# Performance work log

Measured on AMD Instinct MI355X. Metric: run time of the kernel, lower is better.

## Reference

```python
import jax, jax.numpy as jnp
import numpy as np

IMAGE_W = 1024
IMAGE_H = 1024
STRIDES = (8, 16, 32, 64, 128)
TOP_N = 1000
MIN_SCORE = 0.05
NMS_THR = 0.6
MAX_DET = 100
NEG = -1e9  # sentinel for suppressed scores


def _positions(stride):
    # Faithful to repo: shifts_x indexed by feature_h, shifts_y by feature_w,
    # grid built [hf, wf, 2] = [shift_x_i, shift_y_j], then permute(1,0,2).
    hf, wf = IMAGE_H // stride, IMAGE_W // stride
    sx = (jnp.arange(hf, dtype=jnp.float32) + 0.5) * stride
    sy = (jnp.arange(wf, dtype=jnp.float32) + 0.5) * stride
    pos = jnp.stack(jnp.meshgrid(sx, sy, indexing='ij'), axis=-1)  # [hf, wf, 2]
    return jnp.transpose(pos, (1, 0, 2)).reshape(-1, 2)  # [hf*wf, 2]


def _filter_level(cls_h, reg_h, ctr_h, pos):
    B, C = cls_h.shape[0], cls_h.shape[-1]
    cls_h = jax.nn.sigmoid(cls_h).reshape(B, -1, C)
    reg_h = jnp.exp(reg_h).reshape(B, -1, 4)
    ctr_h = jax.nn.sigmoid(ctr_h).reshape(B, -1)
    scores = jnp.max(cls_h, axis=-1)
    classes = jnp.argmax(cls_h, axis=-1).astype(jnp.int32)
    scores = jnp.sqrt(scores * ctr_h)
    N = scores.shape[1]
    if N >= TOP_N:
        scores, idx = jax.lax.top_k(scores, TOP_N)  # sorted descending, like torch.topk
        classes = jnp.take_along_axis(classes, idx, axis=1)
        reg_h = jnp.take_along_axis(reg_h, idx[..., None], axis=1)
        posb = pos[idx]  # [B, TOP_N, 2]
    else:
        posb = jnp.broadcast_to(pos[None], (B, N, 2))
    return scores, classes, reg_h, posb


def _snap(reg, pos):
    # reg: [B, N, 4] (l,t,r,b), pos: [B, N, 2]
    b = jnp.concatenate([pos - reg[:, :, 0:2], pos + reg[:, :, 2:4]], axis=-1)
    b = b.astype(jnp.int32)  # torch .int() truncation
    b = jnp.stack([
        jnp.maximum(b[..., 0], 0),
        jnp.maximum(b[..., 1], 0),
        jnp.minimum(b[..., 2], IMAGE_W - 1),
        jnp.minimum(b[..., 3], IMAGE_H - 1),
    ], axis=-1)
    return b.astype(jnp.float32)


def _nms_image(scores, classes, boxes):
    # scores [N], classes [N] int32, boxes [N,4] float (already snapped to int grid)
    s = jnp.where(scores > MIN_SCORE, scores, NEG)
    x1, y1, x2, y2 = boxes[:, 0], boxes[:, 1], boxes[:, 2], boxes[:, 3]
    areas = (x2 - x1) * (y2 - y1)
    out_s = -jnp.ones((MAX_DET,), jnp.float32)
    out_c = -jnp.ones((MAX_DET,), jnp.float32)
    out_b = -jnp.ones((MAX_DET, 4), jnp.float32)

    def body(i, st):
        s, os_, oc, ob = st
        idx = jnp.argmax(s)            # highest remaining score -> sorted keep order
        ok = s[idx] > MIN_SCORE        # any un-suppressed valid candidate left?
        bb = boxes[idx]
        iw = jnp.clip(jnp.minimum(x2, bb[2]) - jnp.maximum(x1, bb[0]), 0.0)
        ih = jnp.clip(jnp.minimum(y2, bb[3]) - jnp.maximum(y1, bb[1]), 0.0)
        inter = iw * ih
        iou = inter / (areas + areas[idx] - inter + 1e-12)
        s = jnp.where((iou > NMS_THR) & ok, NEG, s)
        s = s.at[idx].set(NEG)
        os_ = os_.at[i].set(jnp.where(ok, scores[idx], -1.0))
        oc = oc.at[i].set(jnp.where(ok, classes[idx].astype(jnp.float32), -1.0))
        ob = ob.at[i].set(jnp.where(ok, bb, -jnp.ones((4,), jnp.float32)))
        return (s, os_, oc, ob)

    _, os_, oc, ob = jax.lax.fori_loop(0, MAX_DET, body, (s, out_s, out_c, out_b))
    return os_, oc, ob


def _decode(cls_heads, reg_heads, ctr_heads):
    sc_l, cl_l, rg_l, ps_l = [], [], [], []
    for c, r, t, st in zip(cls_heads, reg_heads, ctr_heads, STRIDES):
        sc, cl, rg, ps = _filter_level(c, r, t, _positions(st))
        sc_l.append(sc); cl_l.append(cl); rg_l.append(rg); ps_l.append(ps)
    scores = jnp.concatenate(sc_l, axis=1)
    classes = jnp.concatenate(cl_l, axis=1)
    regs = jnp.concatenate(rg_l, axis=1)
    poss = jnp.concatenate(ps_l, axis=1)
    boxes = _snap(regs, poss)
    return jax.vmap(_nms_image)(scores, classes, boxes)


def setup_inputs() -> dict:
    key = jax.random.key(0)
    ks = jax.random.split(key, 15)
    B, C = 8, 80
    sizes = [IMAGE_H // s for s in STRIDES]
    inp = {}
    for i, hw in enumerate(sizes):
        inp[f'cls{i}'] = jax.random.normal(ks[i], (B, hw, hw, C), dtype=jnp.float32)
        # +3 so exp(reg) gives realistic ~20px extents
        inp[f'reg{i}'] = jax.random.normal(ks[5 + i], (B, hw, hw, 4), dtype=jnp.float32) + 3.0
        inp[f'ctr{i}'] = jax.random.normal(ks[10 + i], (B, hw, hw, 1), dtype=jnp.float32)
    return inp


def reference(cls0, cls1, cls2, cls3, cls4,
              reg0, reg1, reg2, reg3, reg4,
              ctr0, ctr1, ctr2, ctr3, ctr4):
    cls_heads = [cls0, cls1, cls2, cls3, cls4]
    reg_heads = [reg0, reg1, reg2, reg3, reg4]
    ctr_heads = [ctr0, ctr1, ctr2, ctr3, ctr4]
    batch_scores, batch_classes, batch_boxes = _decode(cls_heads, reg_heads, ctr_heads)
    return batch_scores, batch_classes, batch_boxes
```

## Files before the change

kernel.cpp:

```cpp
#include <hip/hip_runtime.h>

#define NPOS 21824
#define MINS 0.05f
#define BT2  256
#define NW2  4
#define TFAST 0.85f
#define CAP  16384
#define CNTSTRIDE 32

struct Ptrs { const float* cls[5]; const float* reg[5]; const float* ctr[5]; };

__device__ __forceinline__ float sigf(float x){ return 1.0f/(1.0f+expf(-x)); }

__device__ __forceinline__ void cstore_u32(unsigned* p, unsigned v){
    __hip_atomic_store(p, v, __ATOMIC_RELAXED, __HIP_MEMORY_SCOPE_AGENT);
}
__device__ __forceinline__ void cstore_i32(int* p, int v){
    __hip_atomic_store(p, v, __ATOMIC_RELAXED, __HIP_MEMORY_SCOPE_AGENT);
}
__device__ __forceinline__ void cstore_u64(unsigned long long* p, unsigned long long v){
    __hip_atomic_store(p, v, __ATOMIC_RELAXED, __HIP_MEMORY_SCOPE_AGENT);
}
__device__ __forceinline__ unsigned cload_u32(const unsigned* p){
    return __hip_atomic_load(p, __ATOMIC_RELAXED, __HIP_MEMORY_SCOPE_AGENT);
}
__device__ __forceinline__ int cload_i32(const int* p){
    return __hip_atomic_load(p, __ATOMIC_RELAXED, __HIP_MEMORY_SCOPE_AGENT);
}
__device__ __forceinline__ unsigned long long cload_u64(const unsigned long long* p){
    return __hip_atomic_load(p, __ATOMIC_RELAXED, __HIP_MEMORY_SCOPE_AGENT);
}

__device__ __forceinline__ unsigned long long mkkey(unsigned int b, int p){
    return ((unsigned long long)b << 16) | (unsigned)(65535 - p);
}

__device__ __forceinline__ float4 computeBox(const Ptrs& P, int img, int p){
    int base, lw, stride, lvl;
    if (p < 16384)      { lvl=0; base=0;     lw=7; stride=8;   }
    else if (p < 20480) { lvl=1; base=16384; lw=6; stride=16;  }
    else if (p < 21504) { lvl=2; base=20480; lw=5; stride=32;  }
    else if (p < 21760) { lvl=3; base=21504; lw=4; stride=64;  }
    else                { lvl=4; base=21760; lw=3; stride=128; }
    int pl = p - base;
    int h = pl >> lw, w = pl & ((1<<lw)-1);
    long long lidx = (long long)img*(1<<(2*lw)) + pl;
    float4 rg = ((const float4*)P.reg[lvl])[lidx];
    float x = (w + 0.5f)*(float)stride;
    float y = (h + 0.5f)*(float)stride;
    int ix1 = (int)(x - expf(rg.x));
    int iy1 = (int)(y - expf(rg.y));
    int ix2 = (int)(x + expf(rg.z));
    int iy2 = (int)(y + expf(rg.w));
    ix1 = max(ix1,0); iy1 = max(iy1,0);
    ix2 = min(ix2,1023); iy2 = min(iy2,1023);
    return make_float4((float)ix1,(float)iy1,(float)ix2,(float)iy2);
}

__device__ void suffix_pick(const int* hist, int* wsum, int K,
                            unsigned int prefBase, int shift,
                            unsigned int* shPref, int* shK, int tid)
{
    const int g = 2048 / BT2;
    int lo = tid*g, ls = 0;
#pragma unroll
    for (int q = 0; q < g; ++q) ls += hist[lo + q];
    int lane = tid & 63, wv = tid >> 6;
    int v = ls;
#pragma unroll
    for (int off = 1; off < 64; off <<= 1) {
        int o = __shfl_down(v, off);
        if (lane + off < 64) v += o;
    }
    if (lane == 0) wsum[wv] = v;
    __syncthreads();
    int add = 0;
    for (int q = wv + 1; q < NW2; ++q) add += wsum[q];
    int mine = v + add;
    int above = mine - ls;
    if (above < K && mine >= K) {
        int cum = above;
        for (int b = lo + g - 1; b >= lo; --b) {
            cum += hist[b];
            if (cum >= K) {
                *shPref = prefBase | ((unsigned)b << shift);
                *shK = K - (cum - hist[b]);
                break;
            }
        }
    }
    __syncthreads();
}

__global__ __launch_bounds__(BT2) void k_all(Ptrs P, float* scoreAll, int* clsAll,
                                             unsigned long long* list, int* listCnt,
                                             int* done, float* out)
{
    __shared__ __align__(16) unsigned long long sRow[256][4];
    __shared__ int wsum[NW2];
    __shared__ unsigned int shPref;
    __shared__ int shK, tick, eqn;
    __shared__ unsigned long long eqKey[256];
    __shared__ unsigned long long sel[256];
    __shared__ unsigned long long sorted[256];
    __shared__ float4 sBox[256];
    __shared__ float  sCls[256];
    __shared__ int accIdx[100];
    __shared__ float4 accBox[100];
    __shared__ int shNaM, shNa;
    __shared__ unsigned long long shLast;
    __shared__ int lcnt, lbase, myOrder;

    int* hist = (int*)&sRow[0][0];

    int tid = threadIdx.x;
    int img = blockIdx.y;
    int blk = blockIdx.x;

    {
        int posb = tid >> 2;
        int l    = tid & 3;
        int p    = blk*64 + posb;
        int lvl, base, lw;
        if (blk < 256)      { lvl=0; base=0;     lw=7; }
        else if (blk < 320) { lvl=1; base=16384; lw=6; }
        else if (blk < 336) { lvl=2; base=20480; lw=5; }
        else if (blk < 340) { lvl=3; base=21504; lw=4; }
        else                { lvl=4; base=21760; lw=3; }
        int pl = p - base;
        long long lidx = (long long)img*(1<<(2*lw)) + pl;

        if (tid == 0) lcnt = 0;
        __syncthreads();

        const float4* c4 = (const float4*)(P.cls[lvl] + lidx*80);
        float mx = -3.4e38f; int mi = 0;
#pragma unroll
        for (int j = 0; j < 5; ++j) {
            int k = j*4 + l;
            float4 v = c4[k];
            int cb = k*4;
            if (v.x > mx){mx=v.x; mi=cb;}
            if (v.y > mx){mx=v.y; mi=cb+1;}
            if (v.z > mx){mx=v.z; mi=cb+2;}
            if (v.w > mx){mx=v.w; mi=cb+3;}
        }
#pragma unroll
        for (int d = 1; d < 4; d <<= 1) {
            float omx = __shfl_xor(mx, d);
            int   omi = __shfl_xor(mi, d);
            if (omx > mx || (omx == mx && omi < mi)) { mx = omx; mi = omi; }
        }
        int myTicket = -1;
        unsigned long long myKey = 0;
        if (l == 0) {
            float ct = P.ctr[lvl][lidx];
            float sc = sqrtf(sigf(mx)*sigf(ct));
            int o = img*NPOS + p;
            cstore_u32((unsigned*)scoreAll + o, __float_as_uint(sc));
            cstore_i32(clsAll + o, mi);
            if (sc > TFAST) {
                myTicket = atomicAdd(&lcnt, 1);
                myKey = mkkey(__float_as_uint(sc), p);
            }
        }
        __syncthreads();
        if (tid == 0) lbase = lcnt ? atomicAdd(&listCnt[img*CNTSTRIDE], lcnt) : 0;
        __syncthreads();
        if (myTicket >= 0) {
            int t = lbase + myTicket;
            if (t < CAP) cstore_u64(list + (long long)img*CAP + t, myKey);
        }
    }

    __syncthreads();
    if (tid == 0)
        myOrder = __hip_atomic_fetch_add(&done[img*CNTSTRIDE], 1,
                                         __ATOMIC_RELAXED, __HIP_MEMORY_SCOPE_AGENT);
    __syncthreads();
    if (myOrder != 340) return;

    const unsigned int* gs = (const unsigned int*)scoreAll + (long long)img*NPOS;
    const int* gCls = clsAll + (long long)img*NPOS;
    const unsigned long long* gl = list + (long long)img*CAP;

    float* outS = out + img*100;
    float* outC = out + 800 + img*100;
    float* outB = out + 1600 + img*400;

    int cnt = cload_i32(&listCnt[img*CNTSTRIDE]);
    bool fastPath = (cnt >= 256 && cnt <= CAP);

    for (int i = tid; i < 2048; i += BT2) hist[i] = 0;
    if (tid == 0) { tick = 0; eqn = 0; }
    __syncthreads();

    unsigned int kth; int need;
    if (fastPath) {
        for (int i = tid; i < cnt; i += BT2)
            atomicAdd(&hist[(unsigned)(cload_u64(gl + i) >> 35)], 1);
        __syncthreads();
        suffix_pick(hist, wsum, 256, 0u, 19, &shPref, &shK, tid);
        unsigned int pref = shPref; int K2 = shK;
        for (int i = tid; i < 2048; i += BT2) hist[i] = 0;
        __syncthreads();
        for (int i = tid; i < cnt; i += BT2) {
            unsigned long long k = cload_u64(gl + i);
            if ((unsigned)(k >> 35) == (pref >> 19))
                atomicAdd(&hist[(unsigned)(k >> 24) & 2047], 1);
        }
        __syncthreads();
        suffix_pick(hist, wsum, K2, pref, 8, &shPref, &shK, tid);
        kth = shPref >> 8; need = shK;
        for (int i = tid; i < cnt; i += BT2) {
            unsigned long long k = cload_u64(gl + i);
            unsigned int hb = (unsigned)(k >> 24);
            if (hb > kth)       { int t = atomicAdd(&tick, 1); sel[t] = k; }
            else if (hb == kth) { int t = atomicAdd(&eqn, 1); if (t < 256) eqKey[t] = k; }
        }
    } else {
        for (int i = tid; i < NPOS; i += BT2)
            atomicAdd(&hist[cload_u32(gs + i) >> 19], 1);
        __syncthreads();
        suffix_pick(hist, wsum, 256, 0u, 19, &shPref, &shK, tid);
        unsigned int pref = shPref; int K2 = shK;
        for (int i = tid; i < 2048; i += BT2) hist[i] = 0;
        __syncthreads();
        for (int i = tid; i < NPOS; i += BT2) {
            unsigned int b = cload_u32(gs + i);
            if ((b >> 19) == (pref >> 19)) atomicAdd(&hist[(b >> 8) & 2047], 1);
        }
        __syncthreads();
        suffix_pick(hist, wsum, K2, pref, 8, &shPref, &shK, tid);
        kth = shPref >> 8; need = shK;
        for (int i = tid; i < NPOS; i += BT2) {
            unsigned int b = cload_u32(gs + i), hb = b >> 8;
            if (hb > kth)       { int t = atomicAdd(&tick, 1); sel[t] = mkkey(b, i); }
            else if (hb == kth) { int t = atomicAdd(&eqn, 1); if (t < 256) eqKey[t] = mkkey(b, i); }
        }
    }
    __syncthreads();
    int m = eqn, nG = tick;
    if (m <= 256) {
        for (int q = tid; q < m; q += BT2) {
            unsigned long long kq = eqKey[q];
            int r = 0;
            for (int j = 0; j < m; ++j) r += (eqKey[j] > kq);
            if (r < need) sel[nG + r] = kq;
        }
    } else if (tid == 0) {
        unsigned long long last = ~0ULL;
        for (int c = 0; c < need; ++c) {
            unsigned long long best = 0;
            if (fastPath) {
                for (int i = 0; i < cnt; ++i) {
                    unsigned long long k2 = cload_u64(gl + i);
                    if ((unsigned)(k2 >> 24) == kth && k2 < last && k2 > best) best = k2;
                }
            } else {
                for (int i = 0; i < NPOS; ++i) {
                    unsigned int b = cload_u32(gs + i);
                    if ((b >> 8) == kth) {
                        unsigned long long k2 = mkkey(b, i);
                        if (k2 < last && k2 > best) best = k2;
                    }
                }
            }
            sel[nG + c] = best; last = best;
        }
    }
    __syncthreads();

    {
        unsigned long long k = sel[tid];
        int r = 0;
        for (int j = 0; j < 256; ++j) r += (sel[j] > k);
        sorted[r] = k;
    }
    __syncthreads();
    {
        int p = 65535 - (int)(sorted[tid] & 0xFFFF);
        sBox[tid] = computeBox(P, img, p);
        sCls[tid] = (float)cload_i32(gCls + p);
    }

    float myScore = __uint_as_float((unsigned int)(sorted[tid] >> 16));
    int nValid = __syncthreads_count(myScore > MINS ? 1 : 0);

    {
        float4 bi = sBox[tid];
        float  ai = (bi.z-bi.x)*(bi.w-bi.y);
#pragma unroll
        for (int qq = 0; qq < 4; ++qq) {
            unsigned long long mv = 0;
#pragma unroll 8
            for (int jj = 0; jj < 64; ++jj) {
                int j = qq*64 + jj;
                float4 bj = sBox[j];
                float aj = (bj.z-bj.x)*(bj.w-bj.y);
                float iw = fmaxf(fminf(bj.z,bi.z)-fmaxf(bj.x,bi.x),0.f);
                float ih = fmaxf(fminf(bj.w,bi.w)-fmaxf(bj.y,bi.y),0.f);
                float in_ = iw*ih;
                bool s = (j > tid) && (in_/(aj+ai-in_+1e-12f) > 0.6f);
                mv |= ((unsigned long long)s) << jj;
            }
            sRow[tid][qq] = mv;
        }
    }
    __syncthreads();

    if (tid == 0) {
        int na = 0;
        unsigned long long r0=0, r1=0, r2=0, r3=0;
#define FCOS_WBLK(RW, IB)                                                  \
        {                                                                  \
            int hi = nValid < ((IB)+1)*64 ? nValid : ((IB)+1)*64;          \
            for (int i = (IB)*64; i < hi && na < 100; ++i) {               \
                if ((RW >> (i - (IB)*64)) & 1ull) continue;                \
                accIdx[na++] = i;                                          \
                const ulonglong2* rp = (const ulonglong2*)sRow[i];         \
                ulonglong2 ra = rp[0], rb = rp[1];                         \
                r0 |= ra.x; r1 |= ra.y; r2 |= rb.x; r3 |= rb.y;            \
            }                                                              \
        }
        FCOS_WBLK(r0,0) FCOS_WBLK(r1,1) FCOS_WBLK(r2,2) FCOS_WBLK(r3,3)
#undef FCOS_WBLK
        shNaM = na; shNa = na;
    }
    __syncthreads();

    int naM = shNaM;
    if (naM < 100 && nValid == 256) {
        if (tid < naM) accBox[tid] = sBox[accIdx[tid]];
        if (tid == 0) shLast = sorted[255];
        __syncthreads();
        while (true) {
            if (shNa >= 100) break;
            unsigned long long last = shLast;
            unsigned long long bk = 0;
            for (int i = tid; i < NPOS; i += BT2) {
                unsigned long long k2 = mkkey(cload_u32(gs + i), i);
                if (k2 < last && k2 > bk) bk = k2;
            }
#pragma unroll
            for (int off = 32; off > 0; off >>= 1) {
                unsigned long long o = __shfl_down(bk, off);
                if (o > bk) bk = o;
            }
            int lane = tid & 63, wv = tid >> 6;
            if (lane == 0) eqKey[wv] = bk;
            __syncthreads();
            if (tid == 0) {
                unsigned long long best = 0;
                for (int q = 0; q < NW2; ++q) if (eqKey[q] > best) best = eqKey[q];
                shLast = best;
            }
            __syncthreads();
            unsigned long long ck = shLast;
            if (ck == 0ULL) break;
            float sc = __uint_as_float((unsigned int)(ck >> 16));
            if (!(sc > MINS)) break;
            int p = 65535 - (int)(ck & 0xFFFF);
            float4 bb = computeBox(P, img, p);
            float ba = (bb.z-bb.x)*(bb.w-bb.y);
            int na = shNa;
            bool mySup = false;
            if (tid < na) {
                float4 ab = accBox[tid];
                float aa = (ab.z-ab.x)*(ab.w-ab.y);
                float iw = fmaxf(fminf(bb.z,ab.z)-fmaxf(bb.x,ab.x),0.f);
                float ih = fmaxf(fminf(bb.w,ab.w)-fmaxf(bb.y,ab.y),0.f);
                float in_ = iw*ih;
                mySup = in_/(ba+aa-in_+1e-12f) > 0.6f;
            }
            int supCnt = __syncthreads_count(mySup);
            if (supCnt == 0) {
                if (tid == 0) {
                    int na2 = shNa;
                    outS[na2] = sc;
                    outC[na2] = (float)cload_i32(gCls + p);
                    outB[4*na2+0]=bb.x; outB[4*na2+1]=bb.y;
                    outB[4*na2+2]=bb.z; outB[4*na2+3]=bb.w;
                    accBox[na2] = bb;
                    shNa = na2 + 1;
                }
            }
            __syncthreads();
        }
    }
    __syncthreads();

    {
        int naM2 = shNaM, naT = shNa;
        if (tid < 100) {
            if (tid < naM2) {
                int r = accIdx[tid];
                unsigned long long k = sorted[r];
                float4 b = sBox[r];
                outS[tid] = __uint_as_float((unsigned int)(k >> 16));
                outC[tid] = sCls[r];
                outB[4*tid+0]=b.x; outB[4*tid+1]=b.y;
                outB[4*tid+2]=b.z; outB[4*tid+3]=b.w;
            } else if (tid >= naT) {
                outS[tid] = -1.f; outC[tid] = -1.f;
                outB[4*tid+0]=-1.f; outB[4*tid+1]=-1.f;
                outB[4*tid+2]=-1.f; outB[4*tid+3]=-1.f;
            }
        }
    }
}

extern "C" void kernel_launch(void* const* d_in, const int* in_sizes, int n_in,
                              void* d_out, int out_size, void* d_ws, size_t ws_size,
                              hipStream_t stream) {
    Ptrs P;
    bool interleaved = (in_sizes[1] == 8 * 128 * 128 * 4);
    for (int i = 0; i < 5; ++i) {
        if (interleaved) {
            P.cls[i] = (const float*)d_in[3*i];
            P.reg[i] = (const float*)d_in[3*i + 1];
            P.ctr[i] = (const float*)d_in[3*i + 2];
        } else {
            P.cls[i] = (const float*)d_in[i];
            P.reg[i] = (const float*)d_in[5 + i];
            P.ctr[i] = (const float*)d_in[10 + i];
        }
    }

    char* wbase = (char*)d_ws;
    size_t off = 0;
    auto alloc = [&](size_t bytes) -> void* {
        void* r = wbase + off;
        off += (bytes + 255) & ~(size_t)255;
        return r;
    };
    float*              scoreAll = (float*)alloc((size_t)8 * NPOS * 4);
    int*                clsAll   = (int*)alloc((size_t)8 * NPOS * 4);
    unsigned long long* list     = (unsigned long long*)alloc((size_t)8 * CAP * 8);
    int*                listCnt  = (int*)alloc((size_t)8 * CNTSTRIDE * 4);
    int*                done     = (int*)alloc((size_t)8 * CNTSTRIDE * 4);

    hipMemsetAsync(listCnt, 0, 2 * 8 * CNTSTRIDE * sizeof(int), stream);

    dim3 gA(341, 8);
    k_all<<<gA, BT2, 0, stream>>>(P, scoreAll, clsAll, list, listCnt, done,
                                  (float*)d_out);
}
```

Before: 178.4 us.

## Shard per-image candidate counters and completion tickets into 8 sectors

Splits the single per-image candidate-list counter and done-counter into 8 sector counters (blocks assigned by blk&7), with a two-level completion ticket that picks the last block per image. This is meant to reduce contention on global atomics across the 341 blocks per image. The final block then compacts the sector lists into a shared-memory buffer so the radix-select passes read LDS instead of repeated global atomic loads. Shared-memory buffers are aliased to fit, and the fast path now requires at most 3072 total candidates and 2048 per sector.

```diff
diff --git a/kernel.cpp b/kernel.cpp
--- a/kernel.cpp
+++ b/kernel.cpp
@@ -5,8 +5,11 @@
 #define BT2  256
 #define NW2  4
 #define TFAST 0.85f
-#define CAP  16384
-#define CNTSTRIDE 32
+#define SEC  8
+#define SCAP 2048
+#define CAP  (SEC*SCAP)
+#define SLCAP 3072
+#define CSTRIDE 32
 
 struct Ptrs { const float* cls[5]; const float* reg[5]; const float* ctr[5]; };
 
@@ -93,29 +96,34 @@
 }
 
 __global__ __launch_bounds__(BT2) void k_all(Ptrs P, float* scoreAll, int* clsAll,
-                                             unsigned long long* list, int* listCnt,
-                                             int* done, float* out)
+                                             unsigned long long* list, int* secCnt,
+                                             int* dSec, int* dImg, float* out)
 {
-    __shared__ __align__(16) unsigned long long sRow[256][4];
+    __shared__ __align__(16) unsigned long long slist[SLCAP];
+    __shared__ int hist[2048];
+    __shared__ unsigned long long sel[256];
+    __shared__ unsigned long long eqKey[256];
     __shared__ int wsum[NW2];
+    __shared__ int cntS[SEC], offS[SEC+1];
     __shared__ unsigned int shPref;
     __shared__ int shK, tick, eqn;
-    __shared__ unsigned long long eqKey[256];
-    __shared__ unsigned long long sel[256];
-    __shared__ unsigned long long sorted[256];
-    __shared__ float4 sBox[256];
-    __shared__ float  sCls[256];
-    __shared__ int accIdx[100];
-    __shared__ float4 accBox[100];
-    __shared__ int shNaM, shNa;
+    __shared__ int shNaM, shNa, shTotal, shMaxS;
     __shared__ unsigned long long shLast;
-    __shared__ int lcnt, lbase, myOrder;
-
-    int* hist = (int*)&sRow[0][0];
+    __shared__ int lcnt, lbase, lastFlag;
+
+    unsigned long long* sorted = (unsigned long long*)((char*)slist + 0);
+    float4* sBox  = (float4*)((char*)slist + 2048);
+    float*  sCls  = (float*)((char*)slist + 6144);
+    int*    accIdx= (int*)((char*)slist + 7168);
+    float4* accBox= (float4*)((char*)slist + 7680);
+    unsigned long long (*sRow)[4] =
+        (unsigned long long (*)[4])((char*)slist + 9472);
 
     int tid = threadIdx.x;
     int img = blockIdx.y;
     int blk = blockIdx.x;
+    int s   = blk & 7;
+    int ssz = (s < 5) ? 43 : 42;
 
     {
         int posb = tid >> 2;
@@ -165,20 +173,29 @@
             }
         }
         __syncthreads();
-        if (tid == 0) lbase = lcnt ? atomicAdd(&listCnt[img*CNTSTRIDE], lcnt) : 0;
+        if (tid == 0)
+            lbase = lcnt ? __hip_atomic_fetch_add(&secCnt[(img*SEC+s)*CSTRIDE], lcnt,
+                                __ATOMIC_RELAXED, __HIP_MEMORY_SCOPE_AGENT) : 0;
         __syncthreads();
         if (myTicket >= 0) {
             int t = lbase + myTicket;
-            if (t < CAP) cstore_u64(list + (long long)img*CAP + t, myKey);
-        }
-    }
-
-    __syncthreads();
-    if (tid == 0)
-        myOrder = __hip_atomic_fetch_add(&done[img*CNTSTRIDE], 1,
-                                         __ATOMIC_RELAXED, __HIP_MEMORY_SCOPE_AGENT);
-    __syncthreads();
-    if (myOrder != 340) return;
+            if (t < SCAP) cstore_u64(list + (long long)img*CAP + s*SCAP + t, myKey);
+        }
+    }
+
+    __syncthreads();
+    if (tid == 0) {
+        lastFlag = 0;
+        int t = __hip_atomic_fetch_add(&dSec[(img*SEC+s)*CSTRIDE], 1,
+                                       __ATOMIC_RELAXED, __HIP_MEMORY_SCOPE_AGENT);
+        if (t == ssz - 1) {
+            int t2 = __hip_atomic_fetch_add(&dImg[img*CSTRIDE], 1,
+                                       __ATOMIC_RELAXED, __HIP_MEMORY_SCOPE_AGENT);
+            if (t2 == SEC - 1) lastFlag = 1;
+        }
+    }
+    __syncthreads();
+    if (!lastFlag) return;
 
     const unsigned int* gs = (const unsigned int*)scoreAll + (long long)img*NPOS;
     const int* gCls = clsAll + (long long)img*NPOS;
@@ -188,32 +205,51 @@
     float* outC = out + 800 + img*100;
     float* outB = out + 1600 + img*400;
 
-    int cnt = cload_i32(&listCnt[img*CNTSTRIDE]);
-    bool fastPath = (cnt >= 256 && cnt <= CAP);
-
+    if (tid < SEC) cntS[tid] = cload_i32(&secCnt[(img*SEC+tid)*CSTRIDE]);
+    if (tid == 0) { tick = 0; eqn = 0; }
+    __syncthreads();
+    if (tid == 0) {
+        int o = 0, mx = 0;
+        for (int q = 0; q < SEC; ++q) {
+            offS[q] = o;
+            int c = cntS[q];
+            o += c; if (c > mx) mx = c;
+        }
+        offS[SEC] = o; shTotal = o; shMaxS = mx;
+    }
+    __syncthreads();
+    int total = shTotal;
+    bool fastPath = (total >= 256 && total <= SLCAP && shMaxS <= SCAP);
+
+    if (fastPath) {
+        for (int q = 0; q < SEC; ++q) {
+            int c = cntS[q], o = offS[q];
+            const unsigned long long* seg = gl + q*SCAP;
+            for (int i = tid; i < c; i += BT2) slist[o + i] = cload_u64(seg + i);
+        }
+    }
     for (int i = tid; i < 2048; i += BT2) hist[i] = 0;
-    if (tid == 0) { tick = 0; eqn = 0; }
     __syncthreads();
 
     unsigned int kth; int need;
     if (fastPath) {
-        for (int i = tid; i < cnt; i += BT2)
-            atomicAdd(&hist[(unsigned)(cload_u64(gl + i) >> 35)], 1);
+        for (int i = tid; i < total; i += BT2)
+            atomicAdd(&hist[(unsigned)(slist[i] >> 35)], 1);
         __syncthreads();
         suffix_pick(hist, wsum, 256, 0u, 19, &shPref, &shK, tid);
         unsigned int pref = shPref; int K2 = shK;
         for (int i = tid; i < 2048; i += BT2) hist[i] = 0;
         __syncthreads();
-        for (int i = tid; i < cnt; i += BT2) {
-            unsigned long long k = cload_u64(gl + i);
+        for (int i = tid; i < total; i += BT2) {
+            unsigned long long k = slist[i];
             if ((unsigned)(k >> 35) == (pref >> 19))
                 atomicAdd(&hist[(unsigned)(k >> 24) & 2047], 1);
         }
         __syncthreads();
         suffix_pick(hist, wsum, K2, pref, 8, &shPref, &shK, tid);
         kth = shPref >> 8; need = shK;
-        for (int i = tid; i < cnt; i += BT2) {
-            unsigned long long k = cload_u64(gl + i);
+        for (int i = tid; i < total; i += BT2) {
+            unsigned long long k = slist[i];
             unsigned int hb = (unsigned)(k >> 24);
             if (hb > kth)       { int t = atomicAdd(&tick, 1); sel[t] = k; }
             else if (hb == kth) { int t = atomicAdd(&eqn, 1); if (t < 256) eqKey[t] = k; }
@@ -253,8 +289,8 @@
         for (int c = 0; c < need; ++c) {
             unsigned long long best = 0;
             if (fastPath) {
-                for (int i = 0; i < cnt; ++i) {
-                    unsigned long long k2 = cload_u64(gl + i);
+                for (int i = 0; i < total; ++i) {
+                    unsigned long long k2 = slist[i];
                     if ((unsigned)(k2 >> 24) == kth && k2 < last && k2 > best) best = k2;
                 }
             } else {
@@ -301,8 +337,8 @@
                 float iw = fmaxf(fminf(bj.z,bi.z)-fmaxf(bj.x,bi.x),0.f);
                 float ih = fmaxf(fminf(bj.w,bi.w)-fmaxf(bj.y,bi.y),0.f);
                 float in_ = iw*ih;
-                bool s = (j > tid) && (in_/(aj+ai-in_+1e-12f) > 0.6f);
-                mv |= ((unsigned long long)s) << jj;
+                bool s2 = (j > tid) && (in_/(aj+ai-in_+1e-12f) > 0.6f);
+                mv |= ((unsigned long long)s2) << jj;
             }
             sRow[tid][qq] = mv;
         }
@@ -437,12 +473,14 @@
     float*              scoreAll = (float*)alloc((size_t)8 * NPOS * 4);
     int*                clsAll   = (int*)alloc((size_t)8 * NPOS * 4);
     unsigned long long* list     = (unsigned long long*)alloc((size_t)8 * CAP * 8);
-    int*                listCnt  = (int*)alloc((size_t)8 * CNTSTRIDE * 4);
-    int*                done     = (int*)alloc((size_t)8 * CNTSTRIDE * 4);
-
-    hipMemsetAsync(listCnt, 0, 2 * 8 * CNTSTRIDE * sizeof(int), stream);
+    int*                secCnt   = (int*)alloc((size_t)8 * SEC * CSTRIDE * 4);
+    int*                dSec     = (int*)alloc((size_t)8 * SEC * CSTRIDE * 4);
+    int*                dImg     = (int*)alloc((size_t)8 * CSTRIDE * 4);
+
+    hipMemsetAsync(secCnt, 0,
+                   (size_t)(8*SEC*CSTRIDE + 8*SEC*CSTRIDE + 8*CSTRIDE) * 4, stream);
 
     dim3 gA(341, 8);
-    k_all<<<gA, BT2, 0, stream>>>(P, scoreAll, clsAll, list, listCnt, done,
+    k_all<<<gA, BT2, 0, stream>>>(P, scoreAll, clsAll, list, secCnt, dSec, dImg,
                                   (float*)d_out);
 }
```

Result: faster. 171.2 us (-4.0%).
